# Optimization experiments

Measured on AMD Instinct MI355X. Metric: run time of the kernel, lower is better.

Reference implementation:

```python
import jax, jax.numpy as jnp
import numpy as np

K = 3
PAD = 1
K2 = K * K


def conv2d(x, w, b, pad):
    out = jax.lax.conv_general_dilated(
        x, w, window_strides=(1, 1), padding=((pad, pad), (pad, pad)),
        dimension_numbers=("NCHW", "OIHW", "NCHW"))
    return out + b[None, :, None, None]


def deform_conv2d(x, offset, w, b):
    # x: [B,C,H,W], offset: [B,2*K2,H,W] with (dy,dx) pairs per kernel tap
    B, C, H, W = x.shape
    off = offset.reshape(B, K2, 2, H, W)
    dy, dx = off[:, :, 0], off[:, :, 1]                    # [B,K2,H,W]
    ky = (jnp.arange(K2) // K).astype(x.dtype)[None, :, None, None]
    kx = (jnp.arange(K2) % K).astype(x.dtype)[None, :, None, None]
    hh = jnp.arange(H, dtype=x.dtype)[None, None, :, None]
    ww = jnp.arange(W, dtype=x.dtype)[None, None, None, :]
    py = hh - PAD + ky + dy                                # [B,K2,H,W]
    px = ww - PAD + kx + dx

    y0 = jnp.floor(py)
    x0 = jnp.floor(px)
    wy = py - y0
    wx = px - x0

    xflat = x.reshape(B, C, H * W)

    def gather(yi, xi, wgt):
        # per-corner bilinear term; out-of-bounds corners contribute 0
        valid = (yi >= 0) & (yi < H) & (xi >= 0) & (xi < W)
        yc = jnp.clip(yi, 0, H - 1).astype(jnp.int32)
        xc = jnp.clip(xi, 0, W - 1).astype(jnp.int32)
        idx = (yc * W + xc).reshape(B, K2 * H * W)
        vals = jax.vmap(lambda xf, i: xf[:, i])(xflat, idx)  # [B,C,K2*H*W]
        vals = vals.reshape(B, C, K2, H, W)
        m = (wgt * valid.astype(x.dtype)).reshape(B, 1, K2, H, W)
        return vals * m

    sampled = (gather(y0, x0, (1 - wy) * (1 - wx))
               + gather(y0, x0 + 1, (1 - wy) * wx)
               + gather(y0 + 1, x0, wy * (1 - wx))
               + gather(y0 + 1, x0 + 1, wy * wx))          # [B,C,K2,H,W]

    O = w.shape[0]
    out = jnp.einsum('bckhw,ock->bohw', sampled, w.reshape(O, C, K2))
    return out + b[None, :, None, None]


def setup_inputs() -> dict:
    key = jax.random.key(0)
    k1, k2, k3, k4, k5 = jax.random.split(key, 5)
    B, C, O, H, W = 8, 64, 64, 128, 128
    x = jax.random.normal(k1, (B, C, H, W), dtype=jnp.float32)
    fan_in = C * K * K
    # small offset-conv init so learned offsets stay modest (as at train start)
    w_off = jax.random.normal(k2, (2 * K2, C, 3, 3), dtype=jnp.float32) * 0.01
    b_off = jnp.zeros((2 * K2,), dtype=jnp.float32)
    w_def = jax.random.normal(k3, (O, C, K, K), dtype=jnp.float32) / np.sqrt(fan_in).astype(np.float32)
    b_def = jax.random.normal(k4, (O,), dtype=jnp.float32) * 0.01
    return {"x": x, "w_off": w_off, "b_off": b_off, "w_def": w_def, "b_def": b_def}


def reference(x, w_off, b_off, w_def, b_def):
    offset = conv2d(x, w_off, b_off, pad=1)
    return deform_conv2d(x, offset, w_def, b_def)
```

## Files before the change

### kernel.cpp

```cpp
#include <hip/hip_runtime.h>
#include <hip/hip_bf16.h>

constexpr int B_ = 8, C_ = 64, O_ = 64, H_ = 128, W_ = 128;
constexpr int K2_ = 9, OFFC = 18;
constexpr int NPIX = B_ * H_ * W_;

typedef __attribute__((ext_vector_type(8))) short bf16x8;
typedef __attribute__((ext_vector_type(4))) short bf16x4;
typedef __attribute__((ext_vector_type(4))) float f32x4;
typedef __attribute__((ext_vector_type(2))) float f32x2;

__device__ __forceinline__ unsigned short f2bf(float f) {
    unsigned int u = __float_as_uint(f);
    u += 0x7fffu + ((u >> 16) & 1u);
    return (unsigned short)(u >> 16);
}
__device__ __forceinline__ float bf2f(unsigned short s) {
    return __uint_as_float(((unsigned)s) << 16);
}
__device__ __forceinline__ float tobf_f(float v) {
    return bf2f(f2bf(v));
}
__device__ __forceinline__ short f2bf_s(float f) {
    __hip_bfloat16 t = __float2bfloat16(f);
    return *reinterpret_cast<short*>(&t);
}
__device__ __forceinline__ f32x2 bfpair(unsigned u) {
    f32x2 r;
    r[0] = __uint_as_float(u << 16);
    r[1] = __uint_as_float(u & 0xffff0000u);
    return r;
}

__global__ void k_wprep(const float* __restrict__ w_def,
                        unsigned short* __restrict__ wTfrag) {
    int i = blockIdx.x * 256 + threadIdx.x;
    if (i >= O_ * C_ * K2_) return;
    int f = i >> 9;
    int l = (i >> 3) & 63;
    int j = i & 7;
    int kc = f >> 2, nt = f & 3;
    int oc = nt * 16 + (l & 15);
    int K  = kc * 32 + ((l >> 4) << 3) + j;
    int tap = K >> 6, c = K & 63;
    wTfrag[i] = f2bf(w_def[(size_t)oc * (C_ * K2_) + c * K2_ + tap]);
}

__global__ void k_wprep_off(const float* __restrict__ w_off,
                            unsigned short* __restrict__ wOfrag) {
    int i = blockIdx.x * 256 + threadIdx.x;
    if (i >= 36 * 512) return;
    int f = i >> 9;
    int l = (i >> 3) & 63;
    int j = i & 7;
    int kc = f >> 1, nt = f & 1;
    int oc = nt * 16 + (l & 15);
    int K  = kc * 32 + ((l >> 4) << 3) + j;
    int tap = K >> 6, c = K & 63;
    float v = (oc < OFFC) ? w_off[((size_t)oc * C_ + c) * K2_ + tap] : 0.f;
    wOfrag[i] = f2bf(v);
}

constexpr int QS = 6 * 72 * 32;
constexpr int XS_BYTES = 4 * QS;

__global__ __launch_bounds__(512, 2) void k_fused(const float* __restrict__ x,
                                                  const unsigned short* __restrict__ wOfrag,
                                                  const float* __restrict__ b_off,
                                                  const unsigned short* __restrict__ wTfrag,
                                                  const float* __restrict__ b_def,
                                                  float* __restrict__ out) {
    __shared__ __align__(16) char xs[XS_BYTES];
    __shared__ float offsBuf[128][20];

    int bid = blockIdx.x;
    int swz = (bid & 7) * 128 + (bid >> 3);
    int b  = swz >> 7;
    int rem2 = swz & 127;
    int h  = (rem2 >> 1) << 1;
    int w0 = (rem2 & 1) << 6;

    int tid  = threadIdx.x;
    int lane = tid & 63;
    int wave = tid >> 6;

    {
        int col = tid % 72;
        int rem = tid / 72;
        for (int it = tid; it < 6912; it += 512) {
            int c4  = rem & 15;
            int r   = rem >> 4;
            int y    = h - 2 + r;
            int xcol = w0 - 3 + col;
            bf16x4 pk;
            if (((unsigned)y < (unsigned)H_) && ((unsigned)xcol < (unsigned)W_)) {
                const float* g = x + (((size_t)(b * C_ + c4 * 4) * H_ + y) * W_ + xcol);
                pk[0] = f2bf_s(g[0]);
                pk[1] = f2bf_s(g[H_ * W_]);
                pk[2] = f2bf_s(g[2 * H_ * W_]);
                pk[3] = f2bf_s(g[3 * H_ * W_]);
            } else {
                pk = (bf16x4){0, 0, 0, 0};
            }
            int q0 = c4 >> 2;
            int byte = q0 * QS + ((r * 72 + col) * 32) + (c4 & 3) * 8;
            byte ^= ((col & 7) << 4) ^ (q0 << 5);
            *reinterpret_cast<bf16x4*>(xs + byte) = pk;
            col += 8; rem += 7;
            if (col >= 72) { col -= 72; rem += 1; }
        }
    }
    __syncthreads();

    {
        f32x4 acc2[2];
        acc2[0] = (f32x4){0.f, 0.f, 0.f, 0.f};
        acc2[1] = (f32x4){0.f, 0.f, 0.f, 0.f};
        int g   = lane >> 4;
        int pxr = wave * 16 + (lane & 15);
        int rr  = pxr >> 6, cx = pxr & 63;
        #pragma unroll
        for (int kc = 0; kc < 18; ++kc) {
            int K   = kc * 32 + g * 8;
            int tap = K >> 6, c = K & 63;
            int ky = tap / 3, kx = tap % 3;
            int col = cx + kx + 2;
            int r   = rr + ky + 1;
            int qq  = c >> 4;
            int byte = qq * QS + ((r * 72 + col) * 32) + (c & 15) * 2;
            byte ^= ((col & 7) << 4) ^ (qq << 5);
            bf16x8 a  = *reinterpret_cast<const bf16x8*>(xs + byte);
            bf16x8 b0 = *reinterpret_cast<const bf16x8*>(wOfrag + (((kc * 2 + 0) * 64 + lane) << 3));
            bf16x8 b1 = *reinterpret_cast<const bf16x8*>(wOfrag + (((kc * 2 + 1) * 64 + lane) << 3));
            acc2[0] = __builtin_amdgcn_mfma_f32_16x16x32_bf16(a, b0, acc2[0], 0, 0, 0);
            acc2[1] = __builtin_amdgcn_mfma_f32_16x16x32_bf16(a, b1, acc2[1], 0, 0, 0);
        }
        #pragma unroll
        for (int nt = 0; nt < 2; ++nt) {
            int oc = nt * 16 + (lane & 15);
            if (oc < OFFC) {
                float bo = b_off[oc];
                #pragma unroll
                for (int j = 0; j < 4; ++j) {
                    int px = wave * 16 + ((lane >> 4) << 2) + j;
                    offsBuf[px][oc] = acc2[nt][j] + bo;
                }
            }
        }
    }
    __syncthreads();

    f32x4 acc[4];
    #pragma unroll
    for (int nt = 0; nt < 4; ++nt) acc[nt] = (f32x4){0.f, 0.f, 0.f, 0.f};

    int g    = lane >> 4;
    int rowM = lane & 15;
    int pxw  = (wave << 4) + rowM;
    int prr  = pxw >> 6, pcx = pxw & 63;
    int glo  = (g & 1) << 4;
    int qlo  = g >> 1;
    int qhi  = qlo + 2;
    int baseLo = qlo * QS + glo, baseHi = qhi * QS + glo;
    int xorLo  = qlo << 5,  xorHi  = qhi << 5;

    uint4 cl[2][4], ch[2][4];
    float w00_[2], w01_[2], w10_[2], w11_[2];
    int   y0_[2], x0_[2];
    bool  oow_[2];

#define TAP_ISSUE(kk, ss)                                                                          \
    {                                                                                              \
        float2 dv = *reinterpret_cast<const float2*>(&offsBuf[pxw][2 * (kk)]);                     \
        float py  = (float)(h + prr - 1 + ((kk) / 3)) + dv.x;                                      \
        float pxf = (float)(w0 + pcx - 1 + ((kk) % 3)) + dv.y;                                     \
        float y0f = floorf(py), x0f = floorf(pxf);                                                 \
        float wy = py - y0f, wx = pxf - x0f;                                                       \
        int y0 = (int)y0f, x0 = (int)x0f;                                                          \
        int r0 = y0 - (h - 2), c0 = x0 - (w0 - 3);                                                 \
        oow_[ss] = ((unsigned)r0 >= 5u) | ((unsigned)c0 >= 71u);                                   \
        y0_[ss] = y0; x0_[ss] = x0;                                                                \
        int rc = min(max(r0, 0), 4), cc = min(max(c0, 0), 70);                                     \
        w00_[ss] = (1.f - wy) * (1.f - wx);                                                        \
        w01_[ss] = (1.f - wy) * wx;                                                                \
        w10_[ss] = wy * (1.f - wx);                                                                \
        w11_[ss] = wy * wx;                                                                        \
        int A00 = (rc * 72 + cc) << 5;                                                             \
        int s0 = (cc & 7) << 4;                                                                    \
        int s1 = ((cc + 1) & 7) << 4;                                                              \
        cl[ss][0] = *reinterpret_cast<const uint4*>(xs + ((baseLo + A00)        ^ (s0 ^ xorLo)));  \
        cl[ss][1] = *reinterpret_cast<const uint4*>(xs + ((baseLo + A00 + 32)   ^ (s1 ^ xorLo)));  \
        cl[ss][2] = *reinterpret_cast<const uint4*>(xs + ((baseLo + A00 + 2304) ^ (s0 ^ xorLo)));  \
        cl[ss][3] = *reinterpret_cast<const uint4*>(xs + ((baseLo + A00 + 2336) ^ (s1 ^ xorLo)));  \
        ch[ss][0] = *reinterpret_cast<const uint4*>(xs + ((baseHi + A00)        ^ (s0 ^ xorHi)));  \
        ch[ss][1] = *reinterpret_cast<const uint4*>(xs + ((baseHi + A00 + 32)   ^ (s1 ^ xorHi)));  \
        ch[ss][2] = *reinterpret_cast<const uint4*>(xs + ((baseHi + A00 + 2304) ^ (s0 ^ xorHi)));  \
        ch[ss][3] = *reinterpret_cast<const uint4*>(xs + ((baseHi + A00 + 2336) ^ (s1 ^ xorHi)));  \
    }

#define TAP_CONSUME(kk, ss)                                                                        \
    {                                                                                              \
        bf16x8 B0[4], B1[4];                                                                       \
        _Pragma("unroll")                                                                          \
        for (int nt = 0; nt < 4; ++nt) {                                                           \
            B0[nt] = *reinterpret_cast<const bf16x8*>(                                             \
                wTfrag + ((((2 * (kk) + 0) * 4 + nt) * 64 + lane) << 3));                          \
            B1[nt] = *reinterpret_cast<const bf16x8*>(                                             \
                wTfrag + ((((2 * (kk) + 1) * 4 + nt) * 64 + lane) << 3));                          \
        }                                                                                          \
        float w00 = w00_[ss], w01 = w01_[ss], w10 = w10_[ss], w11 = w11_[ss];                      \
        bf16x8 alo;                                                                                \
        {                                                                                          \
            f32x2 L0 = bfpair(cl[ss][0].x) * w00 + bfpair(cl[ss][1].x) * w01                       \
                     + bfpair(cl[ss][2].x) * w10 + bfpair(cl[ss][3].x) * w11;                      \
            f32x2 L1 = bfpair(cl[ss][0].y) * w00 + bfpair(cl[ss][1].y) * w01                       \
                     + bfpair(cl[ss][2].y) * w10 + bfpair(cl[ss][3].y) * w11;                      \
            f32x2 L2 = bfpair(cl[ss][0].z) * w00 + bfpair(cl[ss][1].z) * w01                       \
                     + bfpair(cl[ss][2].z) * w10 + bfpair(cl[ss][3].z) * w11;                      \
            f32x2 L3 = bfpair(cl[ss][0].w) * w00 + bfpair(cl[ss][1].w) * w01                       \
                     + bfpair(cl[ss][2].w) * w10 + bfpair(cl[ss][3].w) * w11;                      \
            alo[0] = f2bf_s(L0[0]); alo[1] = f2bf_s(L0[1]);                                        \
            alo[2] = f2bf_s(L1[0]); alo[3] = f2bf_s(L1[1]);                                        \
            alo[4] = f2bf_s(L2[0]); alo[5] = f2bf_s(L2[1]);                                        \
            alo[6] = f2bf_s(L3[0]); alo[7] = f2bf_s(L3[1]);                                        \
        }                                                                                          \
        bf16x8 ahi;                                                                                \
        {                                                                                          \
            f32x2 H0 = bfpair(ch[ss][0].x) * w00 + bfpair(ch[ss][1].x) * w01                       \
                     + bfpair(ch[ss][2].x) * w10 + bfpair(ch[ss][3].x) * w11;                      \
            f32x2 H1 = bfpair(ch[ss][0].y) * w00 + bfpair(ch[ss][1].y) * w01                       \
                     + bfpair(ch[ss][2].y) * w10 + bfpair(ch[ss][3].y) * w11;                      \
            f32x2 H2 = bfpair(ch[ss][0].z) * w00 + bfpair(ch[ss][1].z) * w01                       \
                     + bfpair(ch[ss][2].z) * w10 + bfpair(ch[ss][3].z) * w11;                      \
            f32x2 H3 = bfpair(ch[ss][0].w) * w00 + bfpair(ch[ss][1].w) * w01                       \
                     + bfpair(ch[ss][2].w) * w10 + bfpair(ch[ss][3].w) * w11;                      \
            ahi[0] = f2bf_s(H0[0]); ahi[1] = f2bf_s(H0[1]);                                        \
            ahi[2] = f2bf_s(H1[0]); ahi[3] = f2bf_s(H1[1]);                                        \
            ahi[4] = f2bf_s(H2[0]); ahi[5] = f2bf_s(H2[1]);                                        \
            ahi[6] = f2bf_s(H3[0]); ahi[7] = f2bf_s(H3[1]);                                        \
        }                                                                                          \
        if (__any(oow_[ss])) {                                                                     \
            if (oow_[ss]) {                                                                        \
                int y0 = y0_[ss], x0 = x0_[ss];                                                    \
                int y1 = y0 + 1, x1 = x0 + 1;                                                      \
                bool vy0 = (y0 >= 0) & (y0 < H_);                                                  \
                bool vy1 = (y1 >= 0) & (y1 < H_);                                                  \
                bool vx0 = (x0 >= 0) & (x0 < W_);                                                  \
                bool vx1 = (x1 >= 0) & (x1 < W_);                                                  \
                float m00 = (vy0 && vx0) ? w00 : 0.f;                                              \
                float m01 = (vy0 && vx1) ? w01 : 0.f;                                              \
                float m10 = (vy1 && vx0) ? w10 : 0.f;                                              \
                float m11 = (vy1 && vx1) ? w11 : 0.f;                                              \
                int y0c = min(max(y0, 0), H_ - 1), y1c = min(max(y1, 0), H_ - 1);                  \
                int x0c = min(max(x0, 0), W_ - 1), x1c = min(max(x1, 0), W_ - 1);                  \
                int i00 = y0c * W_ + x0c, i01 = y0c * W_ + x1c;                                    \
                int i10 = y1c * W_ + x0c, i11 = y1c * W_ + x1c;                                    \
                const float* cb = x + (size_t)b * C_ * H_ * W_;                                    \
                _Pragma("unroll")                                                                  \
                for (int j = 0; j < 8; ++j) {                                                      \
                    const float* cA = cb + (size_t)((g << 3) + j) * (H_ * W_);                     \
                    const float* cB = cb + (size_t)(32 + (g << 3) + j) * (H_ * W_);                \
                    alo[j] = f2bf_s(m00 * tobf_f(cA[i00]) + m01 * tobf_f(cA[i01])                  \
                                  + m10 * tobf_f(cA[i10]) + m11 * tobf_f(cA[i11]));                \
                    ahi[j] = f2bf_s(m00 * tobf_f(cB[i00]) + m01 * tobf_f(cB[i01])                  \
                                  + m10 * tobf_f(cB[i10]) + m11 * tobf_f(cB[i11]));                \
                }                                                                                  \
            }                                                                                      \
        }                                                                                          \
        _Pragma("unroll")                                                                          \
        for (int nt = 0; nt < 4; ++nt)                                                             \
            acc[nt] = __builtin_amdgcn_mfma_f32_16x16x32_bf16(alo, B0[nt], acc[nt], 0, 0, 0);      \
        _Pragma("unroll")                                                                          \
        for (int nt = 0; nt < 4; ++nt)                                                             \
            acc[nt] = __builtin_amdgcn_mfma_f32_16x16x32_bf16(ahi, B1[nt], acc[nt], 0, 0, 0);      \
    }

    TAP_ISSUE(0, 0)
    TAP_ISSUE(1, 1) TAP_CONSUME(0, 0)
    TAP_ISSUE(2, 0) TAP_CONSUME(1, 1)
    TAP_ISSUE(3, 1) TAP_CONSUME(2, 0)
    TAP_ISSUE(4, 0) TAP_CONSUME(3, 1)
    TAP_ISSUE(5, 1) TAP_CONSUME(4, 0)
    TAP_ISSUE(6, 0) TAP_CONSUME(5, 1)
    TAP_ISSUE(7, 1) TAP_CONSUME(6, 0)
    TAP_ISSUE(8, 0) TAP_CONSUME(7, 1)
    TAP_CONSUME(8, 0)

#undef TAP_ISSUE
#undef TAP_CONSUME

    int pxbase = (wave << 4) + (g << 2);
    int rr = pxbase >> 6, cx = pxbase & 63;
    #pragma unroll
    for (int nt = 0; nt < 4; ++nt) {
        int oc = (nt << 4) + rowM;
        float bz = b_def[oc];
        float4 v;
        v.x = acc[nt][0] + bz;
        v.y = acc[nt][1] + bz;
        v.z = acc[nt][2] + bz;
        v.w = acc[nt][3] + bz;
        float* dst = out + (((size_t)b * O_ + oc) * H_ + h + rr) * W_ + w0 + cx;
        *reinterpret_cast<float4*>(dst) = v;
    }
}

extern "C" void kernel_launch(void* const* d_in, const int* in_sizes, int n_in,
                              void* d_out, int out_size, void* d_ws, size_t ws_size,
                              hipStream_t stream) {
    const float* x     = (const float*)d_in[0];
    const float* w_off = (const float*)d_in[1];
    const float* b_off = (const float*)d_in[2];
    const float* w_def = (const float*)d_in[3];
    const float* b_def = (const float*)d_in[4];
    float* out = (float*)d_out;

    char* ws = (char*)d_ws;
    unsigned short* wTf = (unsigned short*)ws;
    unsigned short* wOf = (unsigned short*)(ws + 73728);

    k_wprep<<<(O_ * C_ * K2_ + 255) / 256, 256, 0, stream>>>(w_def, wTf);
    k_wprep_off<<<(36 * 512 + 255) / 256, 256, 0, stream>>>(w_off, wOf);
    k_fused<<<NPIX / 128, 512, 0, stream>>>(x, wOf, b_off, wTf, b_def, out);
}
```

Baseline: 72.59 us.

## Prefetch weight fragments one tap ahead instead of LDS samples, add MFMA priority

Changes the software pipeline across the nine kernel taps. Before, the LDS corner samples for the next tap were prefetched into registers; now those LDS reads happen inline in each tap, and the global weight fragments for the next tap are double-buffered in registers instead. All nine offset pairs are read from LDS up front, the offset buffer row is padded from 20 to 22 floats, and s_setprio raises wave priority around the MFMA block. The goal is to hide global-load latency of the weights and cut register pressure from buffered samples, at the cost of exposing LDS latency in each tap.

```diff
diff --git a/kernel.cpp b/kernel.cpp
--- a/kernel.cpp
+++ b/kernel.cpp
@@ -71,7 +71,7 @@
                                                   const float* __restrict__ b_def,
                                                   float* __restrict__ out) {
     __shared__ __align__(16) char xs[XS_BYTES];
-    __shared__ float offsBuf[128][20];
+    __shared__ float offsBuf[128][22];
 
     int bid = blockIdx.x;
     int swz = (bid & 7) * 128 + (bid >> 3);
@@ -164,61 +164,56 @@
     int baseLo = qlo * QS + glo, baseHi = qhi * QS + glo;
     int xorLo  = qlo << 5,  xorHi  = qhi << 5;
 
-    uint4 cl[2][4], ch[2][4];
-    float w00_[2], w01_[2], w10_[2], w11_[2];
-    int   y0_[2], x0_[2];
-    bool  oow_[2];
-
-#define TAP_ISSUE(kk, ss)                                                                          \
+    float2 off9[9];
+    #pragma unroll
+    for (int k = 0; k < 9; ++k)
+        off9[k] = *reinterpret_cast<const float2*>(&offsBuf[pxw][2 * k]);
+
+    bf16x8 Bb0[2][4], Bb1[2][4];
+
+#define BLOAD(kk, ss)                                                                              \
     {                                                                                              \
-        float2 dv = *reinterpret_cast<const float2*>(&offsBuf[pxw][2 * (kk)]);                     \
-        float py  = (float)(h + prr - 1 + ((kk) / 3)) + dv.x;                                      \
-        float pxf = (float)(w0 + pcx - 1 + ((kk) % 3)) + dv.y;                                     \
+        _Pragma("unroll")                                                                          \
+        for (int nt = 0; nt < 4; ++nt) {                                                           \
+            Bb0[ss][nt] = *reinterpret_cast<const bf16x8*>(                                        \
+                wTfrag + ((((2 * (kk) + 0) * 4 + nt) * 64 + lane) << 3));                          \
+            Bb1[ss][nt] = *reinterpret_cast<const bf16x8*>(                                        \
+                wTfrag + ((((2 * (kk) + 1) * 4 + nt) * 64 + lane) << 3));                          \
+        }                                                                                          \
+    }
+
+#define TAP(kk, ss)                                                                                \
+    {                                                                                              \
+        float dy = off9[kk].x, dx = off9[kk].y;                                                    \
+        float py  = (float)(h + prr - 1 + ((kk) / 3)) + dy;                                        \
+        float pxf = (float)(w0 + pcx - 1 + ((kk) % 3)) + dx;                                       \
         float y0f = floorf(py), x0f = floorf(pxf);                                                 \
         float wy = py - y0f, wx = pxf - x0f;                                                       \
         int y0 = (int)y0f, x0 = (int)x0f;                                                          \
         int r0 = y0 - (h - 2), c0 = x0 - (w0 - 3);                                                 \
-        oow_[ss] = ((unsigned)r0 >= 5u) | ((unsigned)c0 >= 71u);                                   \
-        y0_[ss] = y0; x0_[ss] = x0;                                                                \
+        bool oow = ((unsigned)r0 >= 5u) | ((unsigned)c0 >= 71u);                                   \
         int rc = min(max(r0, 0), 4), cc = min(max(c0, 0), 70);                                     \
-        w00_[ss] = (1.f - wy) * (1.f - wx);                                                        \
-        w01_[ss] = (1.f - wy) * wx;                                                                \
-        w10_[ss] = wy * (1.f - wx);                                                                \
-        w11_[ss] = wy * wx;                                                                        \
+        float w00 = (1.f - wy) * (1.f - wx);                                                       \
+        float w01 = (1.f - wy) * wx;                                                               \
+        float w10 = wy * (1.f - wx);                                                               \
+        float w11 = wy * wx;                                                                       \
         int A00 = (rc * 72 + cc) << 5;                                                             \
         int s0 = (cc & 7) << 4;                                                                    \
         int s1 = ((cc + 1) & 7) << 4;                                                              \
-        cl[ss][0] = *reinterpret_cast<const uint4*>(xs + ((baseLo + A00)        ^ (s0 ^ xorLo)));  \
-        cl[ss][1] = *reinterpret_cast<const uint4*>(xs + ((baseLo + A00 + 32)   ^ (s1 ^ xorLo)));  \
-        cl[ss][2] = *reinterpret_cast<const uint4*>(xs + ((baseLo + A00 + 2304) ^ (s0 ^ xorLo)));  \
-        cl[ss][3] = *reinterpret_cast<const uint4*>(xs + ((baseLo + A00 + 2336) ^ (s1 ^ xorLo)));  \
-        ch[ss][0] = *reinterpret_cast<const uint4*>(xs + ((baseHi + A00)        ^ (s0 ^ xorHi)));  \
-        ch[ss][1] = *reinterpret_cast<const uint4*>(xs + ((baseHi + A00 + 32)   ^ (s1 ^ xorHi)));  \
-        ch[ss][2] = *reinterpret_cast<const uint4*>(xs + ((baseHi + A00 + 2304) ^ (s0 ^ xorHi)));  \
-        ch[ss][3] = *reinterpret_cast<const uint4*>(xs + ((baseHi + A00 + 2336) ^ (s1 ^ xorHi)));  \
-    }
-
-#define TAP_CONSUME(kk, ss)                                                                        \
-    {                                                                                              \
-        bf16x8 B0[4], B1[4];                                                                       \
-        _Pragma("unroll")                                                                          \
-        for (int nt = 0; nt < 4; ++nt) {                                                           \
-            B0[nt] = *reinterpret_cast<const bf16x8*>(                                             \
-                wTfrag + ((((2 * (kk) + 0) * 4 + nt) * 64 + lane) << 3));                          \
-            B1[nt] = *reinterpret_cast<const bf16x8*>(                                             \
-                wTfrag + ((((2 * (kk) + 1) * 4 + nt) * 64 + lane) << 3));                          \
-        }                                                                                          \
-        float w00 = w00_[ss], w01 = w01_[ss], w10 = w10_[ss], w11 = w11_[ss];                      \
         bf16x8 alo;                                                                                \
         {                                                                                          \
-            f32x2 L0 = bfpair(cl[ss][0].x) * w00 + bfpair(cl[ss][1].x) * w01                       \
-                     + bfpair(cl[ss][2].x) * w10 + bfpair(cl[ss][3].x) * w11;                      \
-            f32x2 L1 = bfpair(cl[ss][0].y) * w00 + bfpair(cl[ss][1].y) * w01                       \
-                     + bfpair(cl[ss][2].y) * w10 + bfpair(cl[ss][3].y) * w11;                      \
-            f32x2 L2 = bfpair(cl[ss][0].z) * w00 + bfpair(cl[ss][1].z) * w01                       \
-                     + bfpair(cl[ss][2].z) * w10 + bfpair(cl[ss][3].z) * w11;                      \
-            f32x2 L3 = bfpair(cl[ss][0].w) * w00 + bfpair(cl[ss][1].w) * w01                       \
-                     + bfpair(cl[ss][2].w) * w10 + bfpair(cl[ss][3].w) * w11;                      \
+            uint4 u00 = *reinterpret_cast<const uint4*>(xs + ((baseLo + A00)        ^ (s0 ^ xorLo))); \
+            uint4 u01 = *reinterpret_cast<const uint4*>(xs + ((baseLo + A00 + 32)   ^ (s1 ^ xorLo))); \
+            uint4 u10 = *reinterpret_cast<const uint4*>(xs + ((baseLo + A00 + 2304) ^ (s0 ^ xorLo))); \
+            uint4 u11 = *reinterpret_cast<const uint4*>(xs + ((baseLo + A00 + 2336) ^ (s1 ^ xorLo))); \
+            f32x2 L0 = bfpair(u00.x) * w00 + bfpair(u01.x) * w01                                   \
+                     + bfpair(u10.x) * w10 + bfpair(u11.x) * w11;                                  \
+            f32x2 L1 = bfpair(u00.y) * w00 + bfpair(u01.y) * w01                                   \
+                     + bfpair(u10.y) * w10 + bfpair(u11.y) * w11;                                  \
+            f32x2 L2 = bfpair(u00.z) * w00 + bfpair(u01.z) * w01                                   \
+                     + bfpair(u10.z) * w10 + bfpair(u11.z) * w11;                                  \
+            f32x2 L3 = bfpair(u00.w) * w00 + bfpair(u01.w) * w01                                   \
+                     + bfpair(u10.w) * w10 + bfpair(u11.w) * w11;                                  \
             alo[0] = f2bf_s(L0[0]); alo[1] = f2bf_s(L0[1]);                                        \
             alo[2] = f2bf_s(L1[0]); alo[3] = f2bf_s(L1[1]);                                        \
             alo[4] = f2bf_s(L2[0]); alo[5] = f2bf_s(L2[1]);                                        \
@@ -226,22 +221,25 @@
         }                                                                                          \
         bf16x8 ahi;                                                                                \
         {                                                                                          \
-            f32x2 H0 = bfpair(ch[ss][0].x) * w00 + bfpair(ch[ss][1].x) * w01                       \
-                     + bfpair(ch[ss][2].x) * w10 + bfpair(ch[ss][3].x) * w11;                      \
-            f32x2 H1 = bfpair(ch[ss][0].y) * w00 + bfpair(ch[ss][1].y) * w01                       \
-                     + bfpair(ch[ss][2].y) * w10 + bfpair(ch[ss][3].y) * w11;                      \
-            f32x2 H2 = bfpair(ch[ss][0].z) * w00 + bfpair(ch[ss][1].z) * w01                       \
-                     + bfpair(ch[ss][2].z) * w10 + bfpair(ch[ss][3].z) * w11;                      \
-            f32x2 H3 = bfpair(ch[ss][0].w) * w00 + bfpair(ch[ss][1].w) * w01                       \
-                     + bfpair(ch[ss][2].w) * w10 + bfpair(ch[ss][3].w) * w11;                      \
+            uint4 u00 = *reinterpret_cast<const uint4*>(xs + ((baseHi + A00)        ^ (s0 ^ xorHi))); \
+            uint4 u01 = *reinterpret_cast<const uint4*>(xs + ((baseHi + A00 + 32)   ^ (s1 ^ xorHi))); \
+            uint4 u10 = *reinterpret_cast<const uint4*>(xs + ((baseHi + A00 + 2304) ^ (s0 ^ xorHi))); \
+            uint4 u11 = *reinterpret_cast<const uint4*>(xs + ((baseHi + A00 + 2336) ^ (s1 ^ xorHi))); \
+            f32x2 H0 = bfpair(u00.x) * w00 + bfpair(u01.x) * w01                                   \
+                     + bfpair(u10.x) * w10 + bfpair(u11.x) * w11;                                  \
+            f32x2 H1 = bfpair(u00.y) * w00 + bfpair(u01.y) * w01                                   \
+                     + bfpair(u10.y) * w10 + bfpair(u11.y) * w11;                                  \
+            f32x2 H2 = bfpair(u00.z) * w00 + bfpair(u01.z) * w01                                   \
+                     + bfpair(u10.z) * w10 + bfpair(u11.z) * w11;                                  \
+            f32x2 H3 = bfpair(u00.w) * w00 + bfpair(u01.w) * w01                                   \
+                     + bfpair(u10.w) * w10 + bfpair(u11.w) * w11;                                  \
             ahi[0] = f2bf_s(H0[0]); ahi[1] = f2bf_s(H0[1]);                                        \
             ahi[2] = f2bf_s(H1[0]); ahi[3] = f2bf_s(H1[1]);                                        \
             ahi[4] = f2bf_s(H2[0]); ahi[5] = f2bf_s(H2[1]);                                        \
             ahi[6] = f2bf_s(H3[0]); ahi[7] = f2bf_s(H3[1]);                                        \
         }                                                                                          \
-        if (__any(oow_[ss])) {                                                                     \
-            if (oow_[ss]) {                                                                        \
-                int y0 = y0_[ss], x0 = x0_[ss];                                                    \
+        if (__any(oow)) {                                                                          \
+            if (oow) {                                                                             \
                 int y1 = y0 + 1, x1 = x0 + 1;                                                      \
                 bool vy0 = (y0 >= 0) & (y0 < H_);                                                  \
                 bool vy1 = (y1 >= 0) & (y1 < H_);                                                  \
@@ -267,27 +265,29 @@
                 }                                                                                  \
             }                                                                                      \
         }                                                                                          \
+        __builtin_amdgcn_s_setprio(1);                                                             \
         _Pragma("unroll")                                                                          \
         for (int nt = 0; nt < 4; ++nt)                                                             \
-            acc[nt] = __builtin_amdgcn_mfma_f32_16x16x32_bf16(alo, B0[nt], acc[nt], 0, 0, 0);      \
+            acc[nt] = __builtin_amdgcn_mfma_f32_16x16x32_bf16(alo, Bb0[ss][nt], acc[nt], 0, 0, 0); \
         _Pragma("unroll")                                                                          \
         for (int nt = 0; nt < 4; ++nt)                                                             \
-            acc[nt] = __builtin_amdgcn_mfma_f32_16x16x32_bf16(ahi, B1[nt], acc[nt], 0, 0, 0);      \
-    }
-
-    TAP_ISSUE(0, 0)
-    TAP_ISSUE(1, 1) TAP_CONSUME(0, 0)
-    TAP_ISSUE(2, 0) TAP_CONSUME(1, 1)
-    TAP_ISSUE(3, 1) TAP_CONSUME(2, 0)
-    TAP_ISSUE(4, 0) TAP_CONSUME(3, 1)
-    TAP_ISSUE(5, 1) TAP_CONSUME(4, 0)
-    TAP_ISSUE(6, 0) TAP_CONSUME(5, 1)
-    TAP_ISSUE(7, 1) TAP_CONSUME(6, 0)
-    TAP_ISSUE(8, 0) TAP_CONSUME(7, 1)
-    TAP_CONSUME(8, 0)
-
-#undef TAP_ISSUE
-#undef TAP_CONSUME
+            acc[nt] = __builtin_amdgcn_mfma_f32_16x16x32_bf16(ahi, Bb1[ss][nt], acc[nt], 0, 0, 0); \
+        __builtin_amdgcn_s_setprio(0);                                                             \
+    }
+
+    BLOAD(0, 0)
+    BLOAD(1, 1) TAP(0, 0)
+    BLOAD(2, 0) TAP(1, 1)
+    BLOAD(3, 1) TAP(2, 0)
+    BLOAD(4, 0) TAP(3, 1)
+    BLOAD(5, 1) TAP(4, 0)
+    BLOAD(6, 0) TAP(5, 1)
+    BLOAD(7, 1) TAP(6, 0)
+    BLOAD(8, 0) TAP(7, 1)
+    TAP(8, 0)
+
+#undef BLOAD
+#undef TAP
 
     int pxbase = (wave << 4) + (g << 2);
     int rr = pxbase >> 6, cx = pxbase & 63;
```

Result: slower. 74.88 us (+3.2%).
